# Performance work log

Measured on AMD Instinct MI355X. Metric: run time of the kernel, lower is better.

Reference implementation:

```python
import jax, jax.numpy as jnp
import numpy as np

N = 50000      # nodes
E = 800000     # edges
D = 256        # hidden_dim (input node features)
A = 128        # attention_dim = attention_ratio * heads
H = 8          # heads
DK = A // H    # 16


def setup_inputs() -> dict:
    key = jax.random.key(0)
    ks = jax.random.split(key, 6)
    x = jax.random.normal(ks[0], (N, D), dtype=jnp.float32)
    # small weight scale keeps exp(pre) well-conditioned (module uses tiny const init)
    Wq = jax.random.normal(ks[1], (A, D), dtype=jnp.float32) * 0.02
    bq = jnp.full((A,), 0.01, dtype=jnp.float32)
    Wk = jax.random.normal(ks[2], (A, D), dtype=jnp.float32) * 0.02
    bk = jnp.full((A,), 0.01, dtype=jnp.float32)
    edge_index = jax.random.randint(ks[3], (2, E), 0, N, dtype=jnp.int32)
    # d0_index[1] holds the two node indices each duplicated edge score scatters to
    d0_index = jax.random.randint(ks[4], (2, 2 * E), 0, N, dtype=jnp.int32)
    return {"x": x, "Wq": Wq, "bq": bq, "Wk": Wk, "bk": bk,
            "edge_index": edge_index, "d0_index": d0_index}


def reference(x, Wq, bq, Wk, bk, edge_index, d0_index):
    # linear projections -> [N, H, DK]
    q = (x @ Wq.T + bq).reshape(N, H, DK)
    k = (x @ Wk.T + bk).reshape(N, H, DK)
    src, dst = edge_index[0], edge_index[1]
    q_i = q[src]   # [E, H, DK]
    k_j = k[dst]
    q_j = q[dst]
    k_i = k[src]
    # symmetrized scaled-dot attention score per edge/head
    pre = 0.5 * jnp.sum(q_i * k_j + q_j * k_i, axis=-1)  # [E, H]
    pre = jnp.mean(pre, axis=-1)                          # [E]
    diagA1 = jnp.exp(pre)
    # duplicate each edge score: (a, a, b, b, ...) == torch (view(-1,1)*ones(E,2)).view(-1)
    edge_score_per_node = jnp.repeat(diagA1, 2)           # [2E]
    diagA0 = jax.ops.segment_sum(edge_score_per_node, d0_index[1], num_segments=N)
    return diagA0, diagA1
```

## Files before the change

### kernel.cpp

```cpp
#include <hip/hip_runtime.h>
#include <hip/hip_bf16.h>

#define N_NODES 50000
#define N_EDGES 800000
#define DIM 256
#define QKDIM 256
#define N_COPIES 8

typedef __bf16 bfrag  __attribute__((ext_vector_type(8)));
typedef __bf16 bf4    __attribute__((ext_vector_type(4)));
typedef float  ffrag  __attribute__((ext_vector_type(4)));
typedef float  f2     __attribute__((ext_vector_type(2)));
typedef float  f4v    __attribute__((ext_vector_type(4)));

#define EP_PITCH 272

__global__ __launch_bounds__(256) void prep_kernel(
    const float* __restrict__ Wq, const float* __restrict__ Wk,
    __bf16* __restrict__ Wb, float* __restrict__ out,
    float* __restrict__ priv, int flag)
{
    const int tid = blockIdx.x * 256 + threadIdx.x;
    const int i = tid * 4;
    if (i < 65536) {
        const float* s = (i < 32768) ? (Wq + i) : (Wk + (i - 32768));
        const float4 v = *(const float4*)s;
        bf4 o;
        o[0] = (__bf16)v.x; o[1] = (__bf16)v.y; o[2] = (__bf16)v.z; o[3] = (__bf16)v.w;
        *(bf4*)(Wb + i) = o;
    }
    if (flag) {
        if (tid < (N_COPIES * N_NODES) / 4)
            ((float4*)priv)[tid] = make_float4(0.f, 0.f, 0.f, 0.f);
    } else {
        if (i + 4 <= N_NODES)
            *(float4*)(out + i) = make_float4(0.f, 0.f, 0.f, 0.f);
    }
}

__global__ __launch_bounds__(256) void proj_mfma(
    const float* __restrict__ x,
    const __bf16* __restrict__ Wb,
    const float* __restrict__ bq, const float* __restrict__ bk,
    unsigned char* __restrict__ qk8)
{
    __shared__ __bf16 As[64 * 256];

    const int tid  = threadIdx.x;
    const int wv   = tid >> 6;
    const int lane = tid & 63;
    const int m    = lane & 15;
    const int q    = lane >> 4;
    const int mbase = blockIdx.x * 64;

    {
        const int srow = tid >> 2;
        const int c4   = tid & 3;
        int grow = mbase + srow;
        grow = grow < N_NODES ? grow : N_NODES - 1;
        const float* xp = x + (size_t)grow * DIM;
        const int mt_ = srow >> 4, m_ = srow & 15;
        #pragma unroll
        for (int i = 0; i < 16; ++i) {
            const int k = c4 * 4 + 16 * i;
            const f4v v = __builtin_nontemporal_load((const f4v*)(xp + k));
            bf4 o;
            o[0] = (__bf16)v[0]; o[1] = (__bf16)v[1];
            o[2] = (__bf16)v[2]; o[3] = (__bf16)v[3];
            const int seg = (k >> 5) * 4 + mt_;
            const int ln  = ((k >> 3) & 3) * 16 + m_;
            *(bf4*)(As + seg * 512 + ln * 8 + (k & 7)) = o;
        }
    }
    __syncthreads();

    ffrag acc[4][4] = {};

    #pragma unroll
    for (int h = 0; h < 2; ++h) {
        bfrag b[4][4];
        #pragma unroll
        for (int sp = 0; sp < 4; ++sp)
            #pragma unroll
            for (int nt = 0; nt < 4; ++nt) {
                const int col = wv * 64 + nt * 16 + m;
                b[sp][nt] = *(const bfrag*)(Wb + (size_t)col * DIM
                                            + 32 * (4 * h + sp) + 8 * q);
            }
        #pragma unroll
        for (int sp = 0; sp < 4; ++sp) {
            bfrag a[4];
            #pragma unroll
            for (int mt = 0; mt < 4; ++mt)
                a[mt] = *(const bfrag*)(As + ((4 * h + sp) * 4 + mt) * 512 + lane * 8);
            #pragma unroll
            for (int mt = 0; mt < 4; ++mt)
                #pragma unroll
                for (int nt = 0; nt < 4; ++nt)
                    acc[mt][nt] = __builtin_amdgcn_mfma_f32_16x16x32_bf16(
                                      a[mt], b[sp][nt], acc[mt][nt], 0, 0, 0);
        }
    }

    __syncthreads();
    unsigned char* ep = (unsigned char*)As;
    #pragma unroll
    for (int nt = 0; nt < 4; ++nt) {
        const int col  = wv * 64 + nt * 16 + m;
        const float bias = (col < 128) ? bq[col] : bk[col - 128];
        #pragma unroll
        for (int mt = 0; mt < 4; ++mt) {
            #pragma unroll
            for (int r = 0; r < 4; ++r) {
                const int rl = mt * 16 + q * 4 + r;
                const float v = acc[mt][nt][r] + bias;
                const int pk = __builtin_amdgcn_cvt_pk_fp8_f32(v, v, 0, false);
                ep[rl * EP_PITCH + col] = (unsigned char)(pk & 0xFF);
            }
        }
    }
    __syncthreads();
    {
        const int rl = tid >> 2;
        const int ch = tid & 3;
        const int grow = mbase + rl;
        if (grow < N_NODES) {
            const uint4* s4 = (const uint4*)(ep + rl * EP_PITCH + ch * 64);
            const uint4 t0 = s4[0], t1 = s4[1], t2 = s4[2], t3 = s4[3];
            uint4* g = (uint4*)(qk8 + (size_t)grow * QKDIM + ch * 64);
            g[0] = t0; g[1] = t1; g[2] = t2; g[3] = t3;
        }
    }
}

__global__ __launch_bounds__(256) void edge_kernel(
    const unsigned char* __restrict__ qk8,
    const int* __restrict__ edge_index,
    const int* __restrict__ d0,
    float* __restrict__ out,
    float* __restrict__ accum, int copymask)
{
    const int wave = (blockIdx.x * blockDim.x + threadIdx.x) >> 6;
    const int lane = threadIdx.x & 63;
    const int g = lane >> 2;
    const int j = lane & 3;
    const int e = wave * 16 + g;

    float* myacc = accum + (size_t)(blockIdx.x & copymask) * N_NODES;

    const int src = __builtin_nontemporal_load(edge_index + e);
    const int dst = __builtin_nontemporal_load(edge_index + N_EDGES + e);

    const uint4* rs = (const uint4*)(qk8 + (size_t)src * QKDIM + 64 * j);
    const uint4* rd = (const uint4*)(qk8 + (size_t)dst * QKDIM + 64 * ((j + 2) & 3));

    uint4 a[4], b[4];
    #pragma unroll
    for (int i = 0; i < 4; ++i) { a[i] = rs[i]; b[i] = rd[i]; }

    f2 acc = {0.f, 0.f};
    #pragma unroll
    for (int i = 0; i < 4; ++i) {
        const unsigned int* ua = (const unsigned int*)&a[i];
        const unsigned int* ub = (const unsigned int*)&b[i];
        #pragma unroll
        for (int t = 0; t < 4; ++t) {
            const f2 x0 = __builtin_amdgcn_cvt_pk_f32_fp8(ua[t], false);
            const f2 y0 = __builtin_amdgcn_cvt_pk_f32_fp8(ub[t], false);
            const f2 x1 = __builtin_amdgcn_cvt_pk_f32_fp8(ua[t], true);
            const f2 y1 = __builtin_amdgcn_cvt_pk_f32_fp8(ub[t], true);
            acc += x0 * y0;
            acc += x1 * y1;
        }
    }
    float p = acc[0] + acc[1];

    p += __shfl_xor(p, 1, 64);
    p += __shfl_xor(p, 2, 64);

    if (j < 2) {
        const float val = __expf(p * 0.0625f);
        const int target = __builtin_nontemporal_load(d0 + 2 * e + j);
        if (j == 0) __builtin_nontemporal_store(val, out + N_NODES + e);
        atomicAdd(&myacc[target], val);
    }
}

__global__ __launch_bounds__(256) void reduce_kernel(
    const float* __restrict__ priv, float* __restrict__ out)
{
    const int idx = (blockIdx.x * 256 + threadIdx.x) * 4;
    if (idx < N_NODES) {
        f4v s = __builtin_nontemporal_load((const f4v*)(priv + idx));
        #pragma unroll
        for (int c = 1; c < N_COPIES; ++c)
            s += __builtin_nontemporal_load((const f4v*)(priv + (size_t)c * N_NODES + idx));
        *(f4v*)(out + idx) = s;
    }
}

extern "C" void kernel_launch(void* const* d_in, const int* in_sizes, int n_in,
                              void* d_out, int out_size, void* d_ws, size_t ws_size,
                              hipStream_t stream) {
    const float* x  = (const float*)d_in[0];
    const float* Wq = (const float*)d_in[1];
    const float* bq = (const float*)d_in[2];
    const float* Wk = (const float*)d_in[3];
    const float* bk = (const float*)d_in[4];
    const int* edge_index = (const int*)d_in[5];
    const int* d0 = (const int*)d_in[6] + 2 * N_EDGES;
    float* out = (float*)d_out;

    unsigned char* qk8 = (unsigned char*)d_ws;
    __bf16* Wb = (__bf16*)((char*)d_ws + (size_t)N_NODES * QKDIM);
    float* priv = (float*)((char*)d_ws + (size_t)N_NODES * QKDIM + 131072);

    const size_t needed = (size_t)N_NODES * QKDIM + 131072
                        + (size_t)N_COPIES * N_NODES * sizeof(float);
    const int use_priv = (ws_size >= needed) ? 1 : 0;
    float* accum = use_priv ? priv : out;
    const int copymask = use_priv ? (N_COPIES - 1) : 0;

    prep_kernel<<<391, 256, 0, stream>>>(Wq, Wk, Wb, out, priv, use_priv);
    proj_mfma<<<(N_NODES + 63) / 64, 256, 0, stream>>>(x, Wb, bq, bk, qk8);

    edge_kernel<<<N_EDGES / 64, 256, 0, stream>>>(qk8, edge_index, d0, out,
                                                  accum, copymask);
    if (use_priv)
        reduce_kernel<<<(N_NODES / 4 + 255) / 256, 256, 0, stream>>>(priv, out);
}
```

Before: 216.4 us.

## Bucket-sort edges by source node block and remap workgroups per XCD

Adds a counting sort (histogram, two scans, scatter) that groups edges by src>>7 into packed records holding src, dst and both scatter targets, plus the original edge id. A sorted edge kernel walks these records, and a block-index remap gives each XCD a contiguous range of buckets. The aim is better L2 locality for the src-row gathers from the fp8 q/k table. The price is four extra launches and the write and re-read of about 16 MB of records on every call. The original edge kernel stays as a fallback when workspace is too small.

```diff
diff --git a/kernel.cpp b/kernel.cpp
--- a/kernel.cpp
+++ b/kernel.cpp
@@ -6,6 +6,9 @@
 #define DIM 256
 #define QKDIM 256
 #define N_COPIES 8
+#define NB 391
+#define NBLK 391
+#define EPB 2048
 
 typedef __bf16 bfrag  __attribute__((ext_vector_type(8)));
 typedef __bf16 bf4    __attribute__((ext_vector_type(4)));
@@ -35,6 +38,89 @@
     } else {
         if (i + 4 <= N_NODES)
             *(float4*)(out + i) = make_float4(0.f, 0.f, 0.f, 0.f);
+    }
+}
+
+__global__ __launch_bounds__(256) void sort_hist(
+    const int* __restrict__ edge_index, int* __restrict__ histg)
+{
+    __shared__ int h[NB];
+    const int tid = threadIdx.x;
+    for (int b = tid; b < NB; b += 256) h[b] = 0;
+    __syncthreads();
+    const int base = blockIdx.x * EPB;
+    #pragma unroll
+    for (int i = 0; i < 8; ++i) {
+        const int e = base + i * 256 + tid;
+        if (e < N_EDGES) atomicAdd(&h[edge_index[e] >> 7], 1);
+    }
+    __syncthreads();
+    for (int b = tid; b < NB; b += 256)
+        histg[b * NBLK + blockIdx.x] = h[b];
+}
+
+__global__ __launch_bounds__(64) void sort_scan_a(
+    const int* __restrict__ histg, int* __restrict__ offs, int* __restrict__ total)
+{
+    const int b = blockIdx.x;
+    const int l = threadIdx.x;
+    int carry = 0;
+    for (int c = 0; c < NBLK; c += 64) {
+        const int idx = c + l;
+        int v = (idx < NBLK) ? histg[b * NBLK + idx] : 0;
+        int s = v;
+        #pragma unroll
+        for (int d = 1; d < 64; d <<= 1) {
+            const int t = __shfl_up(s, d, 64);
+            if (l >= d) s += t;
+        }
+        if (idx < NBLK) offs[b * NBLK + idx] = carry + s - v;
+        carry += __shfl(s, 63, 64);
+    }
+    if (l == 0) total[b] = carry;
+}
+
+__global__ __launch_bounds__(64) void sort_scan_b(
+    const int* __restrict__ total, int* __restrict__ basep)
+{
+    const int l = threadIdx.x;
+    int carry = 0;
+    for (int c = 0; c < NB; c += 64) {
+        const int idx = c + l;
+        int v = (idx < NB) ? total[idx] : 0;
+        int s = v;
+        #pragma unroll
+        for (int d = 1; d < 64; d <<= 1) {
+            const int t = __shfl_up(s, d, 64);
+            if (l >= d) s += t;
+        }
+        if (idx < NB) basep[idx] = carry + s - v;
+        carry += __shfl(s, 63, 64);
+    }
+}
+
+__global__ __launch_bounds__(256) void sort_scatter(
+    const int* __restrict__ edge_index, const int* __restrict__ d0,
+    const int* __restrict__ offs, const int* __restrict__ basep,
+    int4* __restrict__ recA, int* __restrict__ recE)
+{
+    __shared__ int cur[NB];
+    const int tid = threadIdx.x;
+    for (int b = tid; b < NB; b += 256)
+        cur[b] = basep[b] + offs[b * NBLK + blockIdx.x];
+    __syncthreads();
+    const int base = blockIdx.x * EPB;
+    #pragma unroll
+    for (int i = 0; i < 8; ++i) {
+        const int e = base + i * 256 + tid;
+        if (e < N_EDGES) {
+            const int src = edge_index[e];
+            const int dst = edge_index[N_EDGES + e];
+            const int2 t01 = *(const int2*)(d0 + 2 * e);
+            const int pos = atomicAdd(&cur[src >> 7], 1);
+            recA[pos] = make_int4(src, dst, t01.x, t01.y);
+            recE[pos] = e;
+        }
     }
 }
 
@@ -133,23 +219,26 @@
     }
 }
 
-__global__ __launch_bounds__(256) void edge_kernel(
+__global__ __launch_bounds__(256) void edge_kernel_sorted(
     const unsigned char* __restrict__ qk8,
-    const int* __restrict__ edge_index,
-    const int* __restrict__ d0,
-    float* __restrict__ out,
-    float* __restrict__ accum, int copymask)
-{
-    const int wave = (blockIdx.x * blockDim.x + threadIdx.x) >> 6;
+    const int4* __restrict__ recA, const int* __restrict__ recE,
+    float* __restrict__ out, float* __restrict__ accum, int copymask)
+{
+    const int nwg = gridDim.x;
+    const int q8 = nwg >> 3, r8 = nwg & 7;
+    const int xcd = blockIdx.x & 7, sub = blockIdx.x >> 3;
+    const int lb = (xcd < r8 ? xcd * (q8 + 1) : r8 * (q8 + 1) + (xcd - r8) * q8) + sub;
+
     const int lane = threadIdx.x & 63;
+    const int wave = lb * 4 + (threadIdx.x >> 6);
     const int g = lane >> 2;
     const int j = lane & 3;
-    const int e = wave * 16 + g;
+    const int slot = wave * 16 + g;
 
     float* myacc = accum + (size_t)(blockIdx.x & copymask) * N_NODES;
 
-    const int src = __builtin_nontemporal_load(edge_index + e);
-    const int dst = __builtin_nontemporal_load(edge_index + N_EDGES + e);
+    const int4 rec = recA[slot];
+    const int src = rec.x, dst = rec.y;
 
     const uint4* rs = (const uint4*)(qk8 + (size_t)src * QKDIM + 64 * j);
     const uint4* rd = (const uint4*)(qk8 + (size_t)dst * QKDIM + 64 * ((j + 2) & 3));
@@ -174,14 +263,60 @@
         }
     }
     float p = acc[0] + acc[1];
-
     p += __shfl_xor(p, 1, 64);
     p += __shfl_xor(p, 2, 64);
 
     if (j < 2) {
         const float val = __expf(p * 0.0625f);
-        const int target = __builtin_nontemporal_load(d0 + 2 * e + j);
-        if (j == 0) __builtin_nontemporal_store(val, out + N_NODES + e);
+        if (j == 0) out[N_NODES + recE[slot]] = val;
+        atomicAdd(&myacc[j == 0 ? rec.z : rec.w], val);
+    }
+}
+
+__global__ __launch_bounds__(256) void edge_kernel(
+    const unsigned char* __restrict__ qk8,
+    const int* __restrict__ edge_index, const int* __restrict__ d0,
+    float* __restrict__ out, float* __restrict__ accum, int copymask)
+{
+    const int wave = (blockIdx.x * blockDim.x + threadIdx.x) >> 6;
+    const int lane = threadIdx.x & 63;
+    const int g = lane >> 2, j = lane & 3;
+    const int e = wave * 16 + g;
+
+    float* myacc = accum + (size_t)(blockIdx.x & copymask) * N_NODES;
+    const int src = edge_index[e];
+    const int dst = edge_index[N_EDGES + e];
+
+    const uint4* rs = (const uint4*)(qk8 + (size_t)src * QKDIM + 64 * j);
+    const uint4* rd = (const uint4*)(qk8 + (size_t)dst * QKDIM + 64 * ((j + 2) & 3));
+
+    uint4 a[4], b[4];
+    #pragma unroll
+    for (int i = 0; i < 4; ++i) { a[i] = rs[i]; b[i] = rd[i]; }
+
+    f2 acc = {0.f, 0.f};
+    #pragma unroll
+    for (int i = 0; i < 4; ++i) {
+        const unsigned int* ua = (const unsigned int*)&a[i];
+        const unsigned int* ub = (const unsigned int*)&b[i];
+        #pragma unroll
+        for (int t = 0; t < 4; ++t) {
+            const f2 x0 = __builtin_amdgcn_cvt_pk_f32_fp8(ua[t], false);
+            const f2 y0 = __builtin_amdgcn_cvt_pk_f32_fp8(ub[t], false);
+            const f2 x1 = __builtin_amdgcn_cvt_pk_f32_fp8(ua[t], true);
+            const f2 y1 = __builtin_amdgcn_cvt_pk_f32_fp8(ub[t], true);
+            acc += x0 * y0;
+            acc += x1 * y1;
+        }
+    }
+    float p = acc[0] + acc[1];
+    p += __shfl_xor(p, 1, 64);
+    p += __shfl_xor(p, 2, 64);
+
+    if (j < 2) {
+        const float val = __expf(p * 0.0625f);
+        const int target = d0[2 * e + j];
+        if (j == 0) out[N_NODES + e] = val;
         atomicAdd(&myacc[target], val);
     }
 }
@@ -211,21 +346,39 @@
     const int* d0 = (const int*)d_in[6] + 2 * N_EDGES;
     float* out = (float*)d_out;
 
-    unsigned char* qk8 = (unsigned char*)d_ws;
-    __bf16* Wb = (__bf16*)((char*)d_ws + (size_t)N_NODES * QKDIM);
-    float* priv = (float*)((char*)d_ws + (size_t)N_NODES * QKDIM + 131072);
-
-    const size_t needed = (size_t)N_NODES * QKDIM + 131072
-                        + (size_t)N_COPIES * N_NODES * sizeof(float);
-    const int use_priv = (ws_size >= needed) ? 1 : 0;
+    char* w = (char*)d_ws;
+    unsigned char* qk8 = (unsigned char*)w;           w += (size_t)N_NODES * QKDIM;
+    __bf16* Wb = (__bf16*)w;                          w += 131072;
+    float* priv = (float*)w;                          w += (size_t)N_COPIES * N_NODES * 4;
+    int4* recA = (int4*)w;                            w += (size_t)N_EDGES * 16;
+    int* recE = (int*)w;                              w += (size_t)N_EDGES * 4;
+    int* histg = (int*)w;                             w += 611584;
+    int* offs = (int*)w;                              w += 611584;
+    int* total = (int*)w;                             w += 1600;
+    int* basep = (int*)w;                             w += 1600;
+
+    const size_t need_sort = (size_t)(w - (char*)d_ws);
+    const size_t need_priv = (size_t)N_NODES * QKDIM + 131072
+                           + (size_t)N_COPIES * N_NODES * 4;
+    const int use_sort = (ws_size >= need_sort) ? 1 : 0;
+    const int use_priv = (ws_size >= need_priv) ? 1 : 0;
     float* accum = use_priv ? priv : out;
     const int copymask = use_priv ? (N_COPIES - 1) : 0;
 
     prep_kernel<<<391, 256, 0, stream>>>(Wq, Wk, Wb, out, priv, use_priv);
     proj_mfma<<<(N_NODES + 63) / 64, 256, 0, stream>>>(x, Wb, bq, bk, qk8);
 
-    edge_kernel<<<N_EDGES / 64, 256, 0, stream>>>(qk8, edge_index, d0, out,
-                                                  accum, copymask);
+    if (use_sort) {
+        sort_hist<<<NBLK, 256, 0, stream>>>(edge_index, histg);
+        sort_scan_a<<<NB, 64, 0, stream>>>(histg, offs, total);
+        sort_scan_b<<<1, 64, 0, stream>>>(total, basep);
+        sort_scatter<<<NBLK, 256, 0, stream>>>(edge_index, d0, offs, basep, recA, recE);
+        edge_kernel_sorted<<<N_EDGES / 64, 256, 0, stream>>>(qk8, recA, recE, out,
+                                                             accum, copymask);
+    } else {
+        edge_kernel<<<N_EDGES / 64, 256, 0, stream>>>(qk8, edge_index, d0, out,
+                                                      accum, copymask);
+    }
     if (use_priv)
         reduce_kernel<<<(N_NODES / 4 + 255) / 256, 256, 0, stream>>>(priv, out);
 }
```

Result: slower. 258.0 us (+19.2%).
